# Performance work log

Measured on AMD Instinct MI355X. Metric: run time of the kernel, lower is better.

Reference implementation:

```python
import jax, jax.numpy as jnp
import numpy as np

UNITS = 512
M = 8
INPUT_DIM = 512
BATCH = 2048


def setup_inputs() -> dict:
    key = jax.random.key(0)
    ks = jax.random.split(key, 9)
    D, U = INPUT_DIM, UNITS
    fused_dim = D + U
    def glorot(k, shape):
        lim = np.sqrt(6.0 / (shape[0] + shape[1])).astype(np.float32)
        return jax.random.uniform(k, shape, jnp.float32, -lim, lim)
    return {
        "inputs": jax.random.normal(ks[0], (BATCH, D), jnp.float32),
        "elapsed": jax.random.uniform(ks[1], (BATCH, 1), jnp.float32),
        "state": jax.random.normal(ks[2], (BATCH, U * M), jnp.float32),
        "W_r": glorot(ks[3], (fused_dim, U * M)),
        "b_r": jnp.zeros((U * M,), jnp.float32),
        "W_d": glorot(ks[4], (fused_dim, U)),
        "b_d": jnp.zeros((U,), jnp.float32),
        "W_u": glorot(ks[5], (fused_dim, U * M)),
        "b_u": jnp.zeros((U * M,), jnp.float32),
    }


def reference(inputs, elapsed, state, W_r, b_r, W_d, b_d, W_u, b_u):
    B = inputs.shape[0]
    # tau_i = 10**(i/2)  =>  ln_tau_i = i * 0.5 * ln(10)
    ln_tau_table = 0.5 * jnp.log(jnp.float32(10.0)) * jnp.arange(M, dtype=jnp.float32)  # [M]
    tau_table = jnp.exp(ln_tau_table)  # [M]

    h_hat = state.reshape(B, UNITS, M)            # [B, U, M]
    h = h_hat.sum(axis=2)                          # [B, U]
    fused = jnp.concatenate([inputs, h], axis=-1)  # [B, D+U]

    # retrieval gate: softmax over M buckets of -(ln_tau_r - table)^2
    ln_tau_r = (fused @ W_r + b_r).reshape(B, UNITS, M)
    rki = jax.nn.softmax(-jnp.square(ln_tau_r - ln_tau_table), axis=2)
    q_input = jnp.sum(rki * h_hat, axis=2)         # [B, U]

    # detect (candidate) with tanh
    reset_value = jnp.concatenate([inputs, q_input], axis=1)
    qk = jnp.tanh(reset_value @ W_d + b_d)[:, :, None]  # [B, U, 1]

    # update gate
    ln_tau_s = (fused @ W_u + b_u).reshape(B, UNITS, M)
    ski = jax.nn.softmax(-jnp.square(ln_tau_s - ln_tau_table), axis=2)

    # exponential decay per bucket: elapsed [B,1] / tau [M] -> [B, M]
    exp_term = jnp.exp(-elapsed / tau_table)[:, None, :]  # [B, 1, M]
    h_hat_next = ((1.0 - ski) * h_hat + ski * qk) * exp_term  # [B, U, M]

    h_next = h_hat_next.sum(axis=2)                # [B, U]
    return h_next, h_hat_next.reshape(B, UNITS * M)
```

## Files before the change

kernel.cpp:

```cpp
#include <hip/hip_runtime.h>
#include <hip/hip_fp16.h>
#include <cmath>

#define B_SZ 2048
#define D_IN 512
#define U_N  512
#define M_B  8
#define FD   1024
#define NRU  4096
#define NRU2 8192

typedef _Float16 f16x8 __attribute__((ext_vector_type(8)));
typedef float    f32x4 __attribute__((ext_vector_type(4)));

typedef const __attribute__((address_space(1))) void glb_cv;
typedef __attribute__((address_space(3))) void lds_v;

__global__ __launch_bounds__(256) void prep_kernel(
    const float* __restrict__ inputs, const float* __restrict__ state,
    __half* __restrict__ fused, __half* __restrict__ reset)
{
    const int b = blockIdx.x;
    const int t = threadIdx.x;

    const float2 iv = *(const float2*)(inputs + (size_t)b * D_IN + t * 2);
    __half2 hv;
    hv.x = __float2half(iv.x);
    hv.y = __float2half(iv.y);
    *(__half2*)(fused + (size_t)b * FD + t * 2) = hv;
    *(__half2*)(reset + (size_t)b * FD + t * 2) = hv;

    const float4* sp = (const float4*)(state + (size_t)b * NRU + t * 16);
    float4 x0 = sp[0], x1 = sp[1], x2 = sp[2], x3 = sp[3];
    float s0 = (x0.x + x0.y) + (x0.z + x0.w) + (x1.x + x1.y) + (x1.z + x1.w);
    float s1 = (x2.x + x2.y) + (x2.z + x2.w) + (x3.x + x3.y) + (x3.z + x3.w);
    __half2 h2;
    h2.x = __float2half(s0);
    h2.y = __float2half(s1);
    *(__half2*)(fused + (size_t)b * FD + D_IN + t * 2) = h2;
}

__global__ __launch_bounds__(256) void convT_kernel(
    const float* __restrict__ W, __half* __restrict__ Wt, int K, int N)
{
    __shared__ float tile[32][33];
    const int kt = blockIdx.y * 32;
    const int nt = blockIdx.x * 32;
    const int t  = threadIdx.x;
    const int c  = t & 31;
    const int r4 = t >> 5;

#pragma unroll
    for (int i = 0; i < 4; i++) {
        int r = r4 + i * 8;
        tile[r][c] = W[(size_t)(kt + r) * N + nt + c];
    }
    __syncthreads();
#pragma unroll
    for (int i = 0; i < 4; i++) {
        int rr = r4 + i * 8;
        Wt[(size_t)(nt + rr) * K + kt + c] = __float2half(tile[c][rr]);
    }
}

template <int BM, int ACT>
__global__ __launch_bounds__(256) void gemm_lds(
    const __half* __restrict__ A, const __half* __restrict__ Bt,
    const float* __restrict__ biasA, const float* __restrict__ biasB, int nsplit,
    float* __restrict__ C, int Ncols, int K)
{
    __shared__ __align__(16) __half sA[BM][32];
    __shared__ __align__(16) __half sB[128][32];

    const int t    = threadIdx.x;
    const int m0   = blockIdx.y * BM;
    const int n0   = blockIdx.x << 7;
    const int lane = t & 63;
    const int w    = t >> 6;
    const int m16  = lane & 15;
    const int quad = lane >> 4;
    constexpr int MI = BM / 32;
    constexpr int IA = BM / 64;
    const int wm = (w & 1) * (BM / 2);
    const int wn = (w >> 1) << 6;

    f32x4 acc[MI][4];
#pragma unroll
    for (int i = 0; i < MI; i++)
#pragma unroll
        for (int j = 0; j < 4; j++)
#pragma unroll
            for (int r = 0; r < 4; r++) acc[i][j][r] = 0.f;

    const __half* gAp[IA];
    const __half* lAp[IA];
#pragma unroll
    for (int i = 0; i < IA; i++) {
        const int off = w * (BM * 16) + i * 1024 + lane * 16;
        const int row = off >> 6;
        const int kc  = (off & 63) >> 1;
        gAp[i] = A + (size_t)(m0 + row) * K + kc;
        lAp[i] = &sA[0][0] + ((w * (BM * 16) + i * 1024) >> 1);
    }
    const __half* gBp[2];
    const __half* lBp[2];
#pragma unroll
    for (int i = 0; i < 2; i++) {
        const int off = w * 2048 + i * 1024 + lane * 16;
        const int row = off >> 6;
        const int kc  = (off & 63) >> 1;
        gBp[i] = Bt + (size_t)(n0 + row) * K + kc;
        lBp[i] = &sB[0][0] + ((w * 2048 + i * 1024) >> 1);
    }

    for (int kt = 0; kt < K; kt += 32) {
        __syncthreads();
#pragma unroll
        for (int i = 0; i < IA; i++)
            __builtin_amdgcn_global_load_lds((glb_cv*)(gAp[i] + kt), (lds_v*)lAp[i], 16, 0, 0);
#pragma unroll
        for (int i = 0; i < 2; i++)
            __builtin_amdgcn_global_load_lds((glb_cv*)(gBp[i] + kt), (lds_v*)lBp[i], 16, 0, 0);
        __syncthreads();

        f16x8 af[MI], bf[4];
#pragma unroll
        for (int mi = 0; mi < MI; mi++)
            af[mi] = *(const f16x8*)&sA[wm + mi * 16 + m16][quad * 8];
#pragma unroll
        for (int ni = 0; ni < 4; ni++)
            bf[ni] = *(const f16x8*)&sB[wn + ni * 16 + m16][quad * 8];
#pragma unroll
        for (int mi = 0; mi < MI; mi++)
#pragma unroll
            for (int ni = 0; ni < 4; ni++)
                acc[mi][ni] = __builtin_amdgcn_mfma_f32_16x16x32_f16(
                    af[mi], bf[ni], acc[mi][ni], 0, 0, 0);
    }

    const float* bp  = (n0 < nsplit) ? biasA : biasB;
    const int    cb0 = (n0 < nsplit) ? n0 : n0 - nsplit;
#pragma unroll
    for (int mi = 0; mi < MI; mi++) {
#pragma unroll
        for (int ni = 0; ni < 4; ni++) {
            const int ctile = wn + ni * 16 + m16;
            const float bv = bp[cb0 + ctile];
            const int col = n0 + ctile;
#pragma unroll
            for (int r = 0; r < 4; r++) {
                const int row = m0 + wm + mi * 16 + quad * 4 + r;
                float v = acc[mi][ni][r] + bv;
                if (ACT == 1) v = tanhf(v);
                C[(size_t)row * Ncols + col] = v;
            }
        }
    }
}

__global__ __launch_bounds__(256) void gate_r_kernel(
    const float* __restrict__ ln_ru, const float* __restrict__ state,
    __half* __restrict__ reset)
{
    const int idx = blockIdx.x * 256 + threadIdx.x;
    const int b = idx >> 9;
    const int u = idx & 511;

    const float TAB[8] = {0.0f, 1.15129254649702f, 2.30258509299405f,
                          3.45387763949107f, 4.60517018598809f, 5.75646273248511f,
                          6.90775527898214f, 8.05904782547916f};

    const float4* xr = (const float4*)(ln_ru + ((size_t)b * NRU2 + u * 8));
    const float4* hh = (const float4*)(state + ((size_t)b * NRU + u * 8));
    float4 x0 = xr[0], x1 = xr[1];
    float4 h0 = hh[0], h1 = hh[1];
    float x[8] = {x0.x, x0.y, x0.z, x0.w, x1.x, x1.y, x1.z, x1.w};
    float h[8] = {h0.x, h0.y, h0.z, h0.w, h1.x, h1.y, h1.z, h1.w};

    float s[8];
    float mx = -1e30f;
#pragma unroll
    for (int i = 0; i < 8; i++) {
        float d = x[i] - TAB[i];
        s[i] = -d * d;
        mx = fmaxf(mx, s[i]);
    }
    float sum = 0.f, qn = 0.f;
#pragma unroll
    for (int i = 0; i < 8; i++) {
        float e = expf(s[i] - mx);
        sum += e;
        qn += e * h[i];
    }
    float q = qn / sum;
    reset[(size_t)b * FD + D_IN + u] = __float2half(q);
}

__global__ __launch_bounds__(256) void final_kernel(
    const float* __restrict__ ln_ru, const float* __restrict__ state,
    const float* __restrict__ qk, const float* __restrict__ elapsed,
    float* __restrict__ out0, float* __restrict__ out1)
{
    const int idx = blockIdx.x * 256 + threadIdx.x;
    const int b = idx >> 9;
    const int u = idx & 511;

    const float TAB[8] = {0.0f, 1.15129254649702f, 2.30258509299405f,
                          3.45387763949107f, 4.60517018598809f, 5.75646273248511f,
                          6.90775527898214f, 8.05904782547916f};
    const float INV_TAU[8] = {1.0f, 0.316227766016838f, 0.1f, 0.0316227766016838f,
                              0.01f, 0.00316227766016838f, 0.001f, 0.000316227766016838f};

    const float4* xr = (const float4*)(ln_ru + ((size_t)b * NRU2 + 4096 + u * 8));
    const float4* hh = (const float4*)(state + ((size_t)b * NRU + u * 8));
    float4 x0 = xr[0], x1 = xr[1];
    float4 h0 = hh[0], h1 = hh[1];
    float x[8] = {x0.x, x0.y, x0.z, x0.w, x1.x, x1.y, x1.z, x1.w};
    float h[8] = {h0.x, h0.y, h0.z, h0.w, h1.x, h1.y, h1.z, h1.w};

    const float q  = qk[(size_t)b * U_N + u];
    const float el = elapsed[b];

    float s[8];
    float mx = -1e30f;
#pragma unroll
    for (int i = 0; i < 8; i++) {
        float d = x[i] - TAB[i];
        s[i] = -d * d;
        mx = fmaxf(mx, s[i]);
    }
    float e[8];
    float sum = 0.f;
#pragma unroll
    for (int i = 0; i < 8; i++) {
        e[i] = expf(s[i] - mx);
        sum += e[i];
    }
    const float inv_sum = 1.0f / sum;

    float hn[8];
    float acc = 0.f;
#pragma unroll
    for (int i = 0; i < 8; i++) {
        float sk = e[i] * inv_sum;
        float et = expf(-el * INV_TAU[i]);
        hn[i] = ((1.0f - sk) * h[i] + sk * q) * et;
        acc += hn[i];
    }

    float4* o = (float4*)(out1 + ((size_t)b * NRU + u * 8));
    o[0] = make_float4(hn[0], hn[1], hn[2], hn[3]);
    o[1] = make_float4(hn[4], hn[5], hn[6], hn[7]);
    out0[(size_t)b * U_N + u] = acc;
}

extern "C" void kernel_launch(void* const* d_in, const int* in_sizes, int n_in,
                              void* d_out, int out_size, void* d_ws, size_t ws_size,
                              hipStream_t stream)
{
    (void)in_sizes; (void)n_in; (void)out_size; (void)ws_size;

    const float* inputs  = (const float*)d_in[0];
    const float* elapsed = (const float*)d_in[1];
    const float* state   = (const float*)d_in[2];
    const float* W_r     = (const float*)d_in[3];
    const float* b_r     = (const float*)d_in[4];
    const float* W_d     = (const float*)d_in[5];
    const float* b_d     = (const float*)d_in[6];
    const float* W_u     = (const float*)d_in[7];
    const float* b_u     = (const float*)d_in[8];
    float* out = (float*)d_out;

    char* ws = (char*)d_ws;
    __half* fused = (__half*)(ws);
    __half* reset = (__half*)(ws + ((size_t)4  << 20));
    __half* WruT  = (__half*)(ws + ((size_t)8  << 20));
    __half* WdT   = (__half*)(ws + ((size_t)24 << 20));
    float*  ln_ru = (float*) (ws + ((size_t)25 << 20));
    float*  qk    = (float*) (ws + ((size_t)89 << 20));

    prep_kernel<<<B_SZ, 256, 0, stream>>>(inputs, state, fused, reset);
    convT_kernel<<<dim3(NRU / 32, FD / 32), 256, 0, stream>>>(W_r, WruT, FD, NRU);
    convT_kernel<<<dim3(NRU / 32, FD / 32), 256, 0, stream>>>(W_u, WruT + (size_t)NRU * FD, FD, NRU);
    convT_kernel<<<dim3(U_N / 32, FD / 32), 256, 0, stream>>>(W_d, WdT, FD, U_N);

    gemm_lds<128, 0><<<dim3(NRU2 / 128, B_SZ / 128), 256, 0, stream>>>(
        fused, WruT, b_r, b_u, NRU, ln_ru, NRU2, FD);

    gate_r_kernel<<<(B_SZ * U_N) / 256, 256, 0, stream>>>(ln_ru, state, reset);

    gemm_lds<64, 1><<<dim3(U_N / 128, B_SZ / 64), 256, 0, stream>>>(
        reset, WdT, b_d, b_d, 1 << 30, qk, U_N, FD);

    final_kernel<<<(B_SZ * U_N) / 256, 256, 0, stream>>>(ln_ru, state, qk, elapsed, out,
                                                         out + (size_t)B_SZ * U_N);
}
```

Measured before the change: 232.9 us.

## Fuse gate softmax into big GEMM epilogue, store fp16 update gate, merge transposes

The retrieval-gate softmax and q computation, and the update-gate softmax, now run in the epilogue of the large fused GEMM. Tiles are staged through LDS so each lane processes 8 contiguous bucket values. This removes the 64MB fp32 ln_ru round trip and the separate gate_r kernel. The update gate is written as fp16 for final_kernel to read, and the three weight-transpose launches become one. Costs: extra LDS syncs in the epilogue, fp16 precision on ski, and fast __expf.

Measured after the change: 231.2 us. Within noise of the previous version (-0.7%).

```diff
diff --git a/kernel.cpp b/kernel.cpp
--- a/kernel.cpp
+++ b/kernel.cpp
@@ -5,7 +5,6 @@
 #define B_SZ 2048
 #define D_IN 512
 #define U_N  512
-#define M_B  8
 #define FD   1024
 #define NRU  4096
 #define NRU2 8192
@@ -15,6 +14,10 @@
 
 typedef const __attribute__((address_space(1))) void glb_cv;
 typedef __attribute__((address_space(3))) void lds_v;
+
+#define TAB_INIT {0.0f, 1.15129254649702f, 2.30258509299405f, \
+                  3.45387763949107f, 4.60517018598809f, 5.75646273248511f, \
+                  6.90775527898214f, 8.05904782547916f}
 
 __global__ __launch_bounds__(256) void prep_kernel(
     const float* __restrict__ inputs, const float* __restrict__ state,
@@ -40,12 +43,21 @@
     *(__half2*)(fused + (size_t)b * FD + D_IN + t * 2) = h2;
 }
 
-__global__ __launch_bounds__(256) void convT_kernel(
-    const float* __restrict__ W, __half* __restrict__ Wt, int K, int N)
+__global__ __launch_bounds__(256) void convT3_kernel(
+    const float* __restrict__ W_r, const float* __restrict__ W_u,
+    const float* __restrict__ W_d, __half* __restrict__ WruT,
+    __half* __restrict__ WdT)
 {
     __shared__ float tile[32][33];
+    const int bx = blockIdx.x;
+    const float* W;
+    __half* Wt;
+    int N, nt;
+    if (bx < 128)      { W = W_r; Wt = WruT;                        N = NRU; nt = bx * 32; }
+    else if (bx < 256) { W = W_u; Wt = WruT + (size_t)NRU * FD;     N = NRU; nt = (bx - 128) * 32; }
+    else               { W = W_d; Wt = WdT;                         N = U_N; nt = (bx - 256) * 32; }
+
     const int kt = blockIdx.y * 32;
-    const int nt = blockIdx.x * 32;
     const int t  = threadIdx.x;
     const int c  = t & 31;
     const int r4 = t >> 5;
@@ -59,18 +71,21 @@
 #pragma unroll
     for (int i = 0; i < 4; i++) {
         int rr = r4 + i * 8;
-        Wt[(size_t)(nt + rr) * K + kt + c] = __float2half(tile[c][rr]);
-    }
-}
-
-template <int BM, int ACT>
-__global__ __launch_bounds__(256) void gemm_lds(
+        Wt[(size_t)(nt + rr) * FD + kt + c] = __float2half(tile[c][rr]);
+    }
+}
+
+template <int BM, int ACT, int EPI>
+__global__ __launch_bounds__(256) void gemm_k(
     const __half* __restrict__ A, const __half* __restrict__ Bt,
     const float* __restrict__ biasA, const float* __restrict__ biasB, int nsplit,
-    float* __restrict__ C, int Ncols, int K)
-{
-    __shared__ __align__(16) __half sA[BM][32];
-    __shared__ __align__(16) __half sB[128][32];
+    float* __restrict__ C, int Ncols,
+    const float* __restrict__ state, __half* __restrict__ resetw,
+    __half* __restrict__ skibuf, int K)
+{
+    extern __shared__ __align__(16) char smem[];
+    __half* sA = (__half*)smem;
+    __half* sB = (__half*)(smem + BM * 64);
 
     const int t    = threadIdx.x;
     const int m0   = blockIdx.y * BM;
@@ -100,7 +115,7 @@
         const int row = off >> 6;
         const int kc  = (off & 63) >> 1;
         gAp[i] = A + (size_t)(m0 + row) * K + kc;
-        lAp[i] = &sA[0][0] + ((w * (BM * 16) + i * 1024) >> 1);
+        lAp[i] = sA + ((w * (BM * 16) + i * 1024) >> 1);
     }
     const __half* gBp[2];
     const __half* lBp[2];
@@ -110,7 +125,7 @@
         const int row = off >> 6;
         const int kc  = (off & 63) >> 1;
         gBp[i] = Bt + (size_t)(n0 + row) * K + kc;
-        lBp[i] = &sB[0][0] + ((w * 2048 + i * 1024) >> 1);
+        lBp[i] = sB + ((w * 2048 + i * 1024) >> 1);
     }
 
     for (int kt = 0; kt < K; kt += 32) {
@@ -126,10 +141,10 @@
         f16x8 af[MI], bf[4];
 #pragma unroll
         for (int mi = 0; mi < MI; mi++)
-            af[mi] = *(const f16x8*)&sA[wm + mi * 16 + m16][quad * 8];
+            af[mi] = *(const f16x8*)(sA + (wm + mi * 16 + m16) * 32 + quad * 8);
 #pragma unroll
         for (int ni = 0; ni < 4; ni++)
-            bf[ni] = *(const f16x8*)&sB[wn + ni * 16 + m16][quad * 8];
+            bf[ni] = *(const f16x8*)(sB + (wn + ni * 16 + m16) * 32 + quad * 8);
 #pragma unroll
         for (int mi = 0; mi < MI; mi++)
 #pragma unroll
@@ -138,113 +153,120 @@
                     af[mi], bf[ni], acc[mi][ni], 0, 0, 0);
     }
 
-    const float* bp  = (n0 < nsplit) ? biasA : biasB;
-    const int    cb0 = (n0 < nsplit) ? n0 : n0 - nsplit;
-#pragma unroll
-    for (int mi = 0; mi < MI; mi++) {
-#pragma unroll
-        for (int ni = 0; ni < 4; ni++) {
-            const int ctile = wn + ni * 16 + m16;
-            const float bv = bp[cb0 + ctile];
-            const int col = n0 + ctile;
-#pragma unroll
-            for (int r = 0; r < 4; r++) {
-                const int row = m0 + wm + mi * 16 + quad * 4 + r;
-                float v = acc[mi][ni][r] + bv;
-                if (ACT == 1) v = tanhf(v);
-                C[(size_t)row * Ncols + col] = v;
+    if constexpr (EPI == 0) {
+        const float* bp  = (n0 < nsplit) ? biasA : biasB;
+        const int    cb0 = (n0 < nsplit) ? n0 : n0 - nsplit;
+#pragma unroll
+        for (int mi = 0; mi < MI; mi++) {
+#pragma unroll
+            for (int ni = 0; ni < 4; ni++) {
+                const int ctile = wn + ni * 16 + m16;
+                const float bv = bp[cb0 + ctile];
+                const int col = n0 + ctile;
+#pragma unroll
+                for (int r = 0; r < 4; r++) {
+                    const int row = m0 + wm + mi * 16 + quad * 4 + r;
+                    float v = acc[mi][ni][r] + bv;
+                    if (ACT == 1) v = tanhf(v);
+                    C[(size_t)row * Ncols + col] = v;
+                }
             }
         }
-    }
-}
-
-__global__ __launch_bounds__(256) void gate_r_kernel(
-    const float* __restrict__ ln_ru, const float* __restrict__ state,
-    __half* __restrict__ reset)
+    } else {
+        __syncthreads();
+        float* ebuf = (float*)smem + w * (64 * 17);
+        const bool is_r = (n0 < nsplit);
+        const float* bp = is_r ? biasA : biasB;
+        const int cb = (is_r ? n0 : n0 - nsplit) + wn;
+        const float TAB[8] = TAB_INIT;
+
+        for (int ni = 0; ni < 4; ni++) {
+            const float bv = bp[cb + ni * 16 + m16];
+#pragma unroll
+            for (int mi = 0; mi < 4; mi++)
+#pragma unroll
+                for (int r = 0; r < 4; r++)
+                    ebuf[(mi * 16 + quad * 4 + r) * 17 + m16] = acc[mi][ni][r] + bv;
+            __syncthreads();
+
+            const int b = m0 + wm + lane;
+#pragma unroll
+            for (int j = 0; j < 2; j++) {
+                const float* rowp = ebuf + lane * 17 + j * 8;
+                float s[8], e[8];
+                float mx = -1e30f;
+#pragma unroll
+                for (int i = 0; i < 8; i++) {
+                    float d = rowp[i] - TAB[i];
+                    s[i] = -d * d;
+                    mx = fmaxf(mx, s[i]);
+                }
+                float sum = 0.f;
+#pragma unroll
+                for (int i = 0; i < 8; i++) {
+                    e[i] = __expf(s[i] - mx);
+                    sum += e[i];
+                }
+                const int c0 = cb + ni * 16 + j * 8;
+                if (is_r) {
+                    const float4* hh = (const float4*)(state + (size_t)b * NRU + c0);
+                    float4 h0 = hh[0], h1 = hh[1];
+                    float hv[8] = {h0.x, h0.y, h0.z, h0.w, h1.x, h1.y, h1.z, h1.w};
+                    float qn = 0.f;
+#pragma unroll
+                    for (int i = 0; i < 8; i++) qn += e[i] * hv[i];
+                    const float q = qn / sum;
+                    resetw[(size_t)b * FD + D_IN + (c0 >> 3)] = __float2half(q);
+                } else {
+                    const float inv = 1.0f / sum;
+                    __half2 o[4];
+#pragma unroll
+                    for (int i = 0; i < 4; i++) {
+                        o[i].x = __float2half(e[2 * i] * inv);
+                        o[i].y = __float2half(e[2 * i + 1] * inv);
+                    }
+                    *(uint4*)(skibuf + (size_t)b * NRU + c0) = *(uint4*)o;
+                }
+            }
+            __syncthreads();
+        }
+    }
+}
+
+__global__ __launch_bounds__(256) void final_kernel(
+    const __half* __restrict__ skibuf, const float* __restrict__ state,
+    const float* __restrict__ qk, const float* __restrict__ elapsed,
+    float* __restrict__ out0, float* __restrict__ out1)
 {
     const int idx = blockIdx.x * 256 + threadIdx.x;
     const int b = idx >> 9;
     const int u = idx & 511;
 
-    const float TAB[8] = {0.0f, 1.15129254649702f, 2.30258509299405f,
-                          3.45387763949107f, 4.60517018598809f, 5.75646273248511f,
-                          6.90775527898214f, 8.05904782547916f};
-
-    const float4* xr = (const float4*)(ln_ru + ((size_t)b * NRU2 + u * 8));
-    const float4* hh = (const float4*)(state + ((size_t)b * NRU + u * 8));
-    float4 x0 = xr[0], x1 = xr[1];
-    float4 h0 = hh[0], h1 = hh[1];
-    float x[8] = {x0.x, x0.y, x0.z, x0.w, x1.x, x1.y, x1.z, x1.w};
-    float h[8] = {h0.x, h0.y, h0.z, h0.w, h1.x, h1.y, h1.z, h1.w};
-
-    float s[8];
-    float mx = -1e30f;
-#pragma unroll
-    for (int i = 0; i < 8; i++) {
-        float d = x[i] - TAB[i];
-        s[i] = -d * d;
-        mx = fmaxf(mx, s[i]);
-    }
-    float sum = 0.f, qn = 0.f;
-#pragma unroll
-    for (int i = 0; i < 8; i++) {
-        float e = expf(s[i] - mx);
-        sum += e;
-        qn += e * h[i];
-    }
-    float q = qn / sum;
-    reset[(size_t)b * FD + D_IN + u] = __float2half(q);
-}
-
-__global__ __launch_bounds__(256) void final_kernel(
-    const float* __restrict__ ln_ru, const float* __restrict__ state,
-    const float* __restrict__ qk, const float* __restrict__ elapsed,
-    float* __restrict__ out0, float* __restrict__ out1)
-{
-    const int idx = blockIdx.x * 256 + threadIdx.x;
-    const int b = idx >> 9;
-    const int u = idx & 511;
-
-    const float TAB[8] = {0.0f, 1.15129254649702f, 2.30258509299405f,
-                          3.45387763949107f, 4.60517018598809f, 5.75646273248511f,
-                          6.90775527898214f, 8.05904782547916f};
     const float INV_TAU[8] = {1.0f, 0.316227766016838f, 0.1f, 0.0316227766016838f,
                               0.01f, 0.00316227766016838f, 0.001f, 0.000316227766016838f};
 
-    const float4* xr = (const float4*)(ln_ru + ((size_t)b * NRU2 + 4096 + u * 8));
+    const uint4 sr = *(const uint4*)(skibuf + (size_t)b * NRU + u * 8);
+    const __half2* sh = (const __half2*)&sr;
+    float sk[8];
+#pragma unroll
+    for (int i = 0; i < 4; i++) {
+        sk[2 * i]     = __half2float(sh[i].x);
+        sk[2 * i + 1] = __half2float(sh[i].y);
+    }
+
     const float4* hh = (const float4*)(state + ((size_t)b * NRU + u * 8));
-    float4 x0 = xr[0], x1 = xr[1];
     float4 h0 = hh[0], h1 = hh[1];
-    float x[8] = {x0.x, x0.y, x0.z, x0.w, x1.x, x1.y, x1.z, x1.w};
     float h[8] = {h0.x, h0.y, h0.z, h0.w, h1.x, h1.y, h1.z, h1.w};
 
     const float q  = qk[(size_t)b * U_N + u];
     const float el = elapsed[b];
 
-    float s[8];
-    float mx = -1e30f;
-#pragma unroll
-    for (int i = 0; i < 8; i++) {
-        float d = x[i] - TAB[i];
-        s[i] = -d * d;
-        mx = fmaxf(mx, s[i]);
-    }
-    float e[8];
-    float sum = 0.f;
-#pragma unroll
-    for (int i = 0; i < 8; i++) {
-        e[i] = expf(s[i] - mx);
-        sum += e[i];
-    }
-    const float inv_sum = 1.0f / sum;
-
     float hn[8];
     float acc = 0.f;
 #pragma unroll
     for (int i = 0; i < 8; i++) {
-        float sk = e[i] * inv_sum;
-        float et = expf(-el * INV_TAU[i]);
-        hn[i] = ((1.0f - sk) * h[i] + sk * q) * et;
+        const float et = __expf(-el * INV_TAU[i]);
+        hn[i] = ((1.0f - sk[i]) * h[i] + sk[i] * q) * et;
         acc += hn[i];
     }
 
@@ -272,26 +294,22 @@
     float* out = (float*)d_out;
 
     char* ws = (char*)d_ws;
-    __half* fused = (__half*)(ws);
-    __half* reset = (__half*)(ws + ((size_t)4  << 20));
-    __half* WruT  = (__half*)(ws + ((size_t)8  << 20));
-    __half* WdT   = (__half*)(ws + ((size_t)24 << 20));
-    float*  ln_ru = (float*) (ws + ((size_t)25 << 20));
-    float*  qk    = (float*) (ws + ((size_t)89 << 20));
+    __half* fused  = (__half*)(ws);
+    __half* reset  = (__half*)(ws + ((size_t)4  << 20));
+    __half* WruT   = (__half*)(ws + ((size_t)8  << 20));
+    __half* WdT    = (__half*)(ws + ((size_t)24 << 20));
+    __half* skibuf = (__half*)(ws + ((size_t)25 << 20));
+    float*  qk     = (float*) (ws + ((size_t)41 << 20));
 
     prep_kernel<<<B_SZ, 256, 0, stream>>>(inputs, state, fused, reset);
-    convT_kernel<<<dim3(NRU / 32, FD / 32), 256, 0, stream>>>(W_r, WruT, FD, NRU);
-    convT_kernel<<<dim3(NRU / 32, FD / 32), 256, 0, stream>>>(W_u, WruT + (size_t)NRU * FD, FD, NRU);
-    convT_kernel<<<dim3(U_N / 32, FD / 32), 256, 0, stream>>>(W_d, WdT, FD, U_N);
-
-    gemm_lds<128, 0><<<dim3(NRU2 / 128, B_SZ / 128), 256, 0, stream>>>(
-        fused, WruT, b_r, b_u, NRU, ln_ru, NRU2, FD);
-
-    gate_r_kernel<<<(B_SZ * U_N) / 256, 256, 0, stream>>>(ln_ru, state, reset);
-
-    gemm_lds<64, 1><<<dim3(U_N / 128, B_SZ / 64), 256, 0, stream>>>(
-        reset, WdT, b_d, b_d, 1 << 30, qk, U_N, FD);
-
-    final_kernel<<<(B_SZ * U_N) / 256, 256, 0, stream>>>(ln_ru, state, qk, elapsed, out,
+    convT3_kernel<<<dim3(272, FD / 32), 256, 0, stream>>>(W_r, W_u, W_d, WruT, WdT);
+
+    gemm_k<128, 0, 1><<<dim3(NRU2 / 128, B_SZ / 128), 256, 17408, stream>>>(
+        fused, WruT, b_r, b_u, NRU, nullptr, 0, state, reset, skibuf, FD);
+
+    gemm_k<64, 1, 0><<<dim3(U_N / 128, B_SZ / 64), 256, 12288, stream>>>(
+        reset, WdT, b_d, b_d, 1 << 30, qk, U_N, nullptr, nullptr, nullptr, FD);
+
+    final_kernel<<<(B_SZ * U_N) / 256, 256, 0, stream>>>(skibuf, state, qk, elapsed, out,
                                                          out + (size_t)B_SZ * U_N);
 }
```
